# Kernel optimization log

Measured on AMD Instinct MI355X. Metric: run time of the kernel, lower is better.

## Reference

```python
import jax, jax.numpy as jnp
import numpy as np

NUM_HEADS = 6
EPS = 1e-05


def setup_inputs() -> dict:
    key = jax.random.key(0)
    k1, k2, k3 = jax.random.split(key, 3)
    B, N, C = 8, 1024, 384
    x = jax.random.normal(k1, (B, N, C), dtype=jnp.float32)
    Wqkv = jax.random.normal(k2, (3 * C, C), dtype=jnp.float32) * (1.0 / np.sqrt(C))
    Wproj = jax.random.normal(k3, (C, C), dtype=jnp.float32) * (1.0 / np.sqrt(C))
    bproj = jnp.zeros((C,), dtype=jnp.float32)
    alpha = jnp.ones((1, NUM_HEADS, 1, 1), dtype=jnp.float32)
    return {"x": x, "Wqkv": Wqkv, "Wproj": Wproj, "bproj": bproj, "alpha": alpha}


def reference(x, Wqkv, Wproj, bproj, alpha):
    B, N, C = x.shape
    H = NUM_HEADS
    hd = C // H
    scale = hd ** -0.5
    # qkv projection (torch Linear: x @ W^T), split into q,k,v of shape [B,H,N,hd]
    qkv = (x @ Wqkv.T).reshape(B, N, 3, H, hd).transpose(2, 0, 3, 1, 4)
    q, k, v = qkv[0], qkv[1], qkv[2]
    attn = jnp.einsum('bhqd,bhkd->bhqk', q, k) * scale  # [B,H,N,N]
    scalattn = attn / N  # divide by attn.size(3) == N
    a = jax.nn.relu(attn)
    a = a / (jnp.sum(a, axis=-1, keepdims=True) + EPS)
    attn = alpha * a + (1.0 - alpha) * scalattn
    out = jnp.einsum('bhqk,bhkd->bhqd', attn, v)  # [B,H,N,hd]
    out = out.transpose(0, 2, 1, 3).reshape(B, N, C)
    return out @ Wproj.T + bproj
```

## Files before the change

### kernel.cpp

```cpp
#include <hip/hip_runtime.h>
#include <stdint.h>

typedef _Float16 f16;
typedef _Float16 half8 __attribute__((ext_vector_type(8)));
typedef float f32x4 __attribute__((ext_vector_type(4)));

#define MFMA16(A, B, C) __builtin_amdgcn_mfma_f32_16x16x32_f16(A, B, C, 0, 0, 0)

#define GLOAD16(g, l) __builtin_amdgcn_global_load_lds( \
    (const __attribute__((address_space(1))) uint32_t*)(g), \
    (__attribute__((address_space(3))) uint32_t*)(l), 16, 0, 0)

__device__ inline uint32_t packh(f16 a, f16 b) {
    union { f16 h[2]; uint32_t u; } t;
    t.h[0] = a; t.h[1] = b;
    return t.u;
}

#define XE4 786432
#define WQ4 110592
#define WP4 36864

__global__ __launch_bounds__(256) void convert_all(
    const float* __restrict__ x, const float* __restrict__ wq,
    const float* __restrict__ wp, f16* __restrict__ xo,
    f16* __restrict__ wqo, f16* __restrict__ wpo) {
    const int total = XE4 + WQ4 + WP4;
    for (int i = blockIdx.x * blockDim.x + threadIdx.x; i < total;
         i += gridDim.x * blockDim.x) {
        const float* src;
        f16* dst;
        int idx = i;
        if (idx < XE4) { src = x; dst = xo; }
        else if (idx < XE4 + WQ4) { idx -= XE4; src = wq; dst = wqo; }
        else { idx -= XE4 + WQ4; src = wp; dst = wpo; }
        float4 v = ((const float4*)src)[idx];
        union { f16 x[4]; uint2 u; } H;
        H.x[0] = (f16)v.x; H.x[1] = (f16)v.y;
        H.x[2] = (f16)v.z; H.x[3] = (f16)v.w;
        ((uint2*)dst)[idx] = H.u;
    }
}

__global__ __launch_bounds__(256) void qkv_gemm(
    const f16* __restrict__ x16, const f16* __restrict__ w16,
    f16* __restrict__ q_, f16* __restrict__ k_, f16* __restrict__ vt_) {
    __shared__ f16 sA[3][4096], sB[3][4096];
    const int tid = threadIdx.x;
    const int w = tid >> 6, lane = tid & 63;
    const int g = lane >> 4, q = lane & 15;
    const int m0 = blockIdx.x * 128, j0 = blockIdx.y * 128;
    const int wm = (w >> 1) * 64, wn = (w & 1) * 64;
    const bool isV = (j0 >= 768);

    const char* gA = (const char*)x16 + (size_t)m0 * 768;
    const char* gB = (const char*)w16 + (size_t)j0 * 768;
    auto STAGE = [&](int buf, int ks) {
#pragma unroll
        for (int i = 0; i < 2; ++i) {
            const int r0 = 32 * w + i * 16;
            const int row = r0 + (lane >> 2);
            const int chs = ((lane & 3) ^ ((row & 6) >> 1)) << 4;
            GLOAD16(gA + (size_t)row * 768 + ks * 64 + chs, &sA[buf][r0 * 32]);
            GLOAD16(gB + (size_t)row * 768 + ks * 64 + chs, &sB[buf][r0 * 32]);
        }
    };

    f32x4 acc[4][4];
#pragma unroll
    for (int i = 0; i < 4; ++i)
#pragma unroll
        for (int j = 0; j < 4; ++j) acc[i][j] = (f32x4){0.f, 0.f, 0.f, 0.f};

    asm volatile("" ::: "memory");
    STAGE(0, 0);
    STAGE(1, 1);
    for (int ks = 0; ks < 12; ++ks) {
        const int cur = ks % 3;
        __builtin_amdgcn_s_barrier();
        if (ks < 10) {
            STAGE((ks + 2) % 3, ks + 2);
            asm volatile("s_waitcnt vmcnt(8)" ::: "memory");
        } else if (ks == 10) {
            asm volatile("s_waitcnt vmcnt(4)" ::: "memory");
        } else {
            asm volatile("s_waitcnt vmcnt(0)" ::: "memory");
        }
        __builtin_amdgcn_s_barrier();

        half8 am[4], bn[4];
#pragma unroll
        for (int mi = 0; mi < 4; ++mi) {
            const int row = wm + 16 * mi + q;
            const int ch = (g ^ ((row & 6) >> 1)) * 8;
            am[mi] = *(const half8*)&sA[cur][row * 32 + ch];
        }
#pragma unroll
        for (int nj = 0; nj < 4; ++nj) {
            const int row = wn + 16 * nj + q;
            const int ch = (g ^ ((row & 6) >> 1)) * 8;
            bn[nj] = *(const half8*)&sB[cur][row * 32 + ch];
        }
        __builtin_amdgcn_s_setprio(1);
        if (!isV) {
#pragma unroll
            for (int mi = 0; mi < 4; ++mi)
#pragma unroll
                for (int nj = 0; nj < 4; ++nj)
                    acc[mi][nj] = MFMA16(bn[nj], am[mi], acc[mi][nj]);
        } else {
#pragma unroll
            for (int mi = 0; mi < 4; ++mi)
#pragma unroll
                for (int nj = 0; nj < 4; ++nj)
                    acc[mi][nj] = MFMA16(am[mi], bn[nj], acc[mi][nj]);
        }
        __builtin_amdgcn_s_setprio(0);
    }

    if (!isV) {
        const int t = j0 / 384;
        const float sc = (t == 0) ? 0.125f : 1.0f;
        f16* dst = (t == 0) ? q_ : k_;
#pragma unroll
        for (int nj = 0; nj < 4; ++nj) {
            const int jb = j0 + wn + 16 * nj + 4 * g;
            const int h = (jb - t * 384) >> 6, d0 = jb & 63;
#pragma unroll
            for (int mi = 0; mi < 4; ++mi) {
                const int mg = m0 + wm + 16 * mi + q;
                const int b = mg >> 10, n = mg & 1023;
                const size_t base = (size_t)(b * 6 + h) * 65536 + (size_t)n * 64 + d0;
                union { f16 x[4]; uint2 u; } H;
#pragma unroll
                for (int r = 0; r < 4; ++r) H.x[r] = (f16)(acc[mi][nj][r] * sc);
                *(uint2*)&dst[base] = H.u;
            }
        }
    } else {
#pragma unroll
        for (int nj = 0; nj < 4; ++nj) {
            const int jc = j0 + wn + 16 * nj + q;
            const int h = (jc - 768) >> 6, d = jc & 63;
#pragma unroll
            for (int mi = 0; mi < 4; ++mi) {
                const int mg = m0 + wm + 16 * mi + 4 * g;
                const int b = mg >> 10, n = mg & 1023;
                const size_t bh = (size_t)(b * 6 + h);
                union { f16 x[4]; uint2 u; } HV;
#pragma unroll
                for (int r = 0; r < 4; ++r) HV.x[r] = (f16)acc[mi][nj][r];
                *(uint2*)&vt_[bh * 65536 + (size_t)d * 1024 + n] = HV.u;
            }
        }
    }
}

__global__ __launch_bounds__(512) void attn_mfma(
    const f16* __restrict__ q_, const f16* __restrict__ k_,
    const f16* __restrict__ vt_, const float* __restrict__ alpha,
    f16* __restrict__ ao_) {
    __shared__ f16 sK[2][4096], sV[2][4096];
    const int tid = threadIdx.x;
    const int w = tid >> 6, lane = tid & 63;
    const int g = lane >> 4, q = lane & 15;
    const int bh = blockIdx.x % 48, h = bh % 6;
    const int n0 = (blockIdx.x / 48) * 128;

    const size_t kbb = (size_t)bh * 131072;
    const int rl8 = lane >> 3, cl8 = lane & 7;

    auto STAGE = [&](int buf, int kt) {
        const size_t kb = kbb + (size_t)kt * 8192;
        const size_t vb = kbb + (size_t)kt * 128;
        const int rloc = 8 * w + rl8;
        const int chs = (cl8 ^ (rloc & 7)) << 4;
        const int ldso = 8 * w * 64;
        GLOAD16((const char*)k_ + kb + (size_t)rloc * 128 + chs, &sK[buf][ldso]);
        GLOAD16((const char*)vt_ + vb + (size_t)rloc * 2048 + chs, &sV[buf][ldso]);
    };

    const size_t qbase = (size_t)bh * 65536 + (size_t)(n0 + 16 * w + q) * 64;
    half8 Qh[2];
    Qh[0] = *(const half8*)&q_[qbase + g * 8];
    Qh[1] = *(const half8*)&q_[qbase + 32 + g * 8];
    const float al = alpha[h];
    const float cg = (1.0f - al) * (1.0f / 1024.0f);
    const bool useLin = (cg != 0.0f);

    f32x4 accP[4], accS[4];
#pragma unroll
    for (int i = 0; i < 4; ++i) {
        accP[i] = (f32x4){0.f, 0.f, 0.f, 0.f};
        accS[i] = (f32x4){0.f, 0.f, 0.f, 0.f};
    }
    float rs = 0.f;

    asm volatile("" ::: "memory");
    STAGE(0, 0);
    int cur = 0;
    for (int kt = 0; kt < 16; ++kt) {
        __builtin_amdgcn_s_barrier();
        if (kt < 15) {
            STAGE(cur ^ 1, kt + 1);
            asm volatile("s_waitcnt vmcnt(2)" ::: "memory");
        } else {
            asm volatile("s_waitcnt vmcnt(0)" ::: "memory");
        }
        __builtin_amdgcn_s_barrier();

        f32x4 sv[4];
        __builtin_amdgcn_s_setprio(1);
#pragma unroll
        for (int s = 0; s < 4; ++s) {
            f32x4 sa = (f32x4){0.f, 0.f, 0.f, 0.f};
            const int row = 16 * s + q;
#pragma unroll
            for (int k2 = 0; k2 < 2; ++k2) {
                const int ch = ((k2 * 4 + g) ^ (row & 7)) * 8;
                half8 kf = *(const half8*)&sK[cur][row * 64 + ch];
                sa = MFMA16(kf, Qh[k2], sa);
            }
            sv[s] = sa;
        }
        __builtin_amdgcn_s_setprio(0);

        uint32_t pk[4][2];
#pragma unroll
        for (int s = 0; s < 4; ++s) {
            float p0 = fmaxf(sv[s][0], 0.f), p1 = fmaxf(sv[s][1], 0.f);
            float p2 = fmaxf(sv[s][2], 0.f), p3 = fmaxf(sv[s][3], 0.f);
            rs += (p0 + p1) + (p2 + p3);
            pk[s][0] = packh((f16)p0, (f16)p1);
            pk[s][1] = packh((f16)p2, (f16)p3);
        }

#pragma unroll
        for (int t2 = 0; t2 < 2; ++t2) {
            union { uint32_t u[4]; half8 v; } fh;
#pragma unroll
            for (int r = 0; r < 4; ++r) {
                const int srcl = ((2 * g + (r >> 1)) & 3) * 16 + q;
                uint32_t a0 = __shfl(pk[2 * t2][r & 1], srcl, 64);
                uint32_t b0 = __shfl(pk[2 * t2 + 1][r & 1], srcl, 64);
                fh.u[r] = (g < 2) ? a0 : b0;
            }
            __builtin_amdgcn_s_setprio(1);
#pragma unroll
            for (int ds = 0; ds < 4; ++ds) {
                const int row = 16 * ds + q;
                const int ch = ((t2 * 4 + g) ^ (row & 7)) * 8;
                half8 vf = *(const half8*)&sV[cur][row * 64 + ch];
                accP[ds] = MFMA16(vf, fh.v, accP[ds]);
            }
            __builtin_amdgcn_s_setprio(0);
        }

        if (useLin) {
            uint32_t sk[4][2];
#pragma unroll
            for (int s = 0; s < 4; ++s) {
                sk[s][0] = packh((f16)sv[s][0], (f16)sv[s][1]);
                sk[s][1] = packh((f16)sv[s][2], (f16)sv[s][3]);
            }
#pragma unroll
            for (int t2 = 0; t2 < 2; ++t2) {
                union { uint32_t u[4]; half8 v; } fh;
#pragma unroll
                for (int r = 0; r < 4; ++r) {
                    const int srcl = ((2 * g + (r >> 1)) & 3) * 16 + q;
                    uint32_t a0 = __shfl(sk[2 * t2][r & 1], srcl, 64);
                    uint32_t b0 = __shfl(sk[2 * t2 + 1][r & 1], srcl, 64);
                    fh.u[r] = (g < 2) ? a0 : b0;
                }
#pragma unroll
                for (int ds = 0; ds < 4; ++ds) {
                    const int row = 16 * ds + q;
                    const int ch = ((t2 * 4 + g) ^ (row & 7)) * 8;
                    half8 vf = *(const half8*)&sV[cur][row * 64 + ch];
                    accS[ds] = MFMA16(vf, fh.v, accS[ds]);
                }
            }
        }
        cur ^= 1;
    }

    rs += __shfl_xor(rs, 16, 64);
    rs += __shfl_xor(rs, 32, 64);
    const float inv = al / (rs + 1e-5f);

    const int b = bh / 6;
    const size_t arow = (size_t)(b * 1024 + n0 + 16 * w + q) * 384 + h * 64;
#pragma unroll
    for (int ds = 0; ds < 4; ++ds) {
        const int d0 = 16 * ds + 4 * g;
        union { f16 x[4]; uint2 u; } H;
#pragma unroll
        for (int r = 0; r < 4; ++r)
            H.x[r] = (f16)(accP[ds][r] * inv + cg * accS[ds][r]);
        *(uint2*)&ao_[arow + d0] = H.u;
    }
}

__global__ __launch_bounds__(256) void proj_gemm(
    const f16* __restrict__ a_, const f16* __restrict__ wp16,
    const float* __restrict__ bias, float* __restrict__ out) {
    __shared__ f16 sA[3][2048], sB[3][4096];
    const int tid = threadIdx.x;
    const int w = tid >> 6, lane = tid & 63;
    const int g = lane >> 4, q = lane & 15;
    const int m0 = blockIdx.x * 64, j0 = blockIdx.y * 128;
    const int wm = (w >> 1) * 32, wn = (w & 1) * 64;

    const char* gA = (const char*)a_ + (size_t)m0 * 768;
    const char* gB = (const char*)wp16 + (size_t)j0 * 768;
    auto STAGE = [&](int buf, int ks) {
        {
            const int r0 = 16 * w;
            const int row = r0 + (lane >> 2);
            const int chs = ((lane & 3) ^ ((row & 6) >> 1)) << 4;
            GLOAD16(gA + (size_t)row * 768 + ks * 64 + chs, &sA[buf][r0 * 32]);
        }
#pragma unroll
        for (int i = 0; i < 2; ++i) {
            const int r0 = 32 * w + i * 16;
            const int row = r0 + (lane >> 2);
            const int chs = ((lane & 3) ^ ((row & 6) >> 1)) << 4;
            GLOAD16(gB + (size_t)row * 768 + ks * 64 + chs, &sB[buf][r0 * 32]);
        }
    };

    f32x4 acc[2][4];
#pragma unroll
    for (int i = 0; i < 2; ++i)
#pragma unroll
        for (int j = 0; j < 4; ++j) acc[i][j] = (f32x4){0.f, 0.f, 0.f, 0.f};

    asm volatile("" ::: "memory");
    STAGE(0, 0);
    STAGE(1, 1);
    for (int ks = 0; ks < 12; ++ks) {
        const int cur = ks % 3;
        __builtin_amdgcn_s_barrier();
        if (ks < 10) {
            STAGE((ks + 2) % 3, ks + 2);
            asm volatile("s_waitcnt vmcnt(6)" ::: "memory");
        } else if (ks == 10) {
            asm volatile("s_waitcnt vmcnt(3)" ::: "memory");
        } else {
            asm volatile("s_waitcnt vmcnt(0)" ::: "memory");
        }
        __builtin_amdgcn_s_barrier();

        half8 am[2], bn[4];
#pragma unroll
        for (int mi = 0; mi < 2; ++mi) {
            const int row = wm + 16 * mi + q;
            const int ch = (g ^ ((row & 6) >> 1)) * 8;
            am[mi] = *(const half8*)&sA[cur][row * 32 + ch];
        }
#pragma unroll
        for (int nj = 0; nj < 4; ++nj) {
            const int row = wn + 16 * nj + q;
            const int ch = (g ^ ((row & 6) >> 1)) * 8;
            bn[nj] = *(const half8*)&sB[cur][row * 32 + ch];
        }
        __builtin_amdgcn_s_setprio(1);
#pragma unroll
        for (int mi = 0; mi < 2; ++mi)
#pragma unroll
            for (int nj = 0; nj < 4; ++nj)
                acc[mi][nj] = MFMA16(bn[nj], am[mi], acc[mi][nj]);
        __builtin_amdgcn_s_setprio(0);
    }

#pragma unroll
    for (int nj = 0; nj < 4; ++nj) {
        const int jb = j0 + wn + 16 * nj + 4 * g;
        const float4 bb = *(const float4*)&bias[jb];
#pragma unroll
        for (int mi = 0; mi < 2; ++mi) {
            const int m = m0 + wm + 16 * mi + q;
            float4 o;
            o.x = acc[mi][nj][0] + bb.x;
            o.y = acc[mi][nj][1] + bb.y;
            o.z = acc[mi][nj][2] + bb.z;
            o.w = acc[mi][nj][3] + bb.w;
            *(float4*)&out[(size_t)m * 384 + jb] = o;
        }
    }
}

extern "C" void kernel_launch(void* const* d_in, const int* in_sizes, int n_in,
                              void* d_out, int out_size, void* d_ws, size_t ws_size,
                              hipStream_t stream) {
    const float* x     = (const float*)d_in[0];
    const float* Wqkv  = (const float*)d_in[1];
    const float* Wproj = (const float*)d_in[2];
    const float* bproj = (const float*)d_in[3];
    const float* alpha = (const float*)d_in[4];
    float* out = (float*)d_out;

    f16* ws = (f16*)d_ws;
    const size_t XE = 8192 * 384;
    const size_t WQ = 1152 * 384;
    const size_t WP = 384 * 384;
    const size_t QE = 48 * 1024 * 64;

    f16* x16  = ws;            f16* wq16 = x16 + XE;
    f16* wp16 = wq16 + WQ;
    f16* qv   = wp16 + WP;     f16* kv   = qv + QE;
    f16* vt   = kv + QE;       f16* ao   = vt + QE;

    convert_all<<<1024, 256, 0, stream>>>(x, Wqkv, Wproj, x16, wq16, wp16);
    qkv_gemm<<<dim3(64, 9), 256, 0, stream>>>(x16, wq16, qv, kv, vt);
    attn_mfma<<<384, 512, 0, stream>>>(qv, kv, vt, alpha, ao);
    proj_gemm<<<dim3(128, 3), 256, 0, stream>>>(ao, wp16, bproj, out);
}
```

Baseline: 134.9 us.

## Switch QKV and proj GEMMs to BK=64 double-buffered pipeline

Both GEMMs move from a 3-stage pipeline with a 32-wide K step to a 2-stage pipeline with a 64-wide K step. The LDS swizzle changes to an 8-chunk XOR pattern to match. This halves the number of barrier pairs and loop iterations per tile and doubles the MFMA work between syncs. The cost is shallower prefetch depth, which may leave more global-load latency exposed, plus more registers for the operand fragments.

```diff
diff --git a/kernel.cpp b/kernel.cpp
--- a/kernel.cpp
+++ b/kernel.cpp
@@ -45,7 +45,7 @@
 __global__ __launch_bounds__(256) void qkv_gemm(
     const f16* __restrict__ x16, const f16* __restrict__ w16,
     f16* __restrict__ q_, f16* __restrict__ k_, f16* __restrict__ vt_) {
-    __shared__ f16 sA[3][4096], sB[3][4096];
+    __shared__ f16 sA[2][8192], sB[2][8192];
     const int tid = threadIdx.x;
     const int w = tid >> 6, lane = tid & 63;
     const int g = lane >> 4, q = lane & 15;
@@ -57,12 +57,12 @@
     const char* gB = (const char*)w16 + (size_t)j0 * 768;
     auto STAGE = [&](int buf, int ks) {
 #pragma unroll
-        for (int i = 0; i < 2; ++i) {
-            const int r0 = 32 * w + i * 16;
-            const int row = r0 + (lane >> 2);
-            const int chs = ((lane & 3) ^ ((row & 6) >> 1)) << 4;
-            GLOAD16(gA + (size_t)row * 768 + ks * 64 + chs, &sA[buf][r0 * 32]);
-            GLOAD16(gB + (size_t)row * 768 + ks * 64 + chs, &sB[buf][r0 * 32]);
+        for (int i = 0; i < 4; ++i) {
+            const int r0 = 32 * w + i * 8;
+            const int row = r0 + (lane >> 3);
+            const int chs = ((lane & 7) ^ (row & 7)) << 4;
+            GLOAD16(gA + (size_t)row * 768 + ks * 128 + chs, &sA[buf][r0 * 64]);
+            GLOAD16(gB + (size_t)row * 768 + ks * 128 + chs, &sB[buf][r0 * 64]);
         }
     };
 
@@ -74,32 +74,35 @@
 
     asm volatile("" ::: "memory");
     STAGE(0, 0);
-    STAGE(1, 1);
-    for (int ks = 0; ks < 12; ++ks) {
-        const int cur = ks % 3;
-        __builtin_amdgcn_s_barrier();
-        if (ks < 10) {
-            STAGE((ks + 2) % 3, ks + 2);
+    int cur = 0;
+    for (int ks = 0; ks < 6; ++ks) {
+        __builtin_amdgcn_s_barrier();
+        if (ks < 5) {
+            STAGE(cur ^ 1, ks + 1);
             asm volatile("s_waitcnt vmcnt(8)" ::: "memory");
-        } else if (ks == 10) {
-            asm volatile("s_waitcnt vmcnt(4)" ::: "memory");
         } else {
             asm volatile("s_waitcnt vmcnt(0)" ::: "memory");
         }
         __builtin_amdgcn_s_barrier();
 
-        half8 am[4], bn[4];
+        half8 am[4][2], bn[4][2];
 #pragma unroll
         for (int mi = 0; mi < 4; ++mi) {
             const int row = wm + 16 * mi + q;
-            const int ch = (g ^ ((row & 6) >> 1)) * 8;
-            am[mi] = *(const half8*)&sA[cur][row * 32 + ch];
+#pragma unroll
+            for (int k2 = 0; k2 < 2; ++k2) {
+                const int ch = ((k2 * 4 + g) ^ (row & 7)) * 8;
+                am[mi][k2] = *(const half8*)&sA[cur][row * 64 + ch];
+            }
         }
 #pragma unroll
         for (int nj = 0; nj < 4; ++nj) {
             const int row = wn + 16 * nj + q;
-            const int ch = (g ^ ((row & 6) >> 1)) * 8;
-            bn[nj] = *(const half8*)&sB[cur][row * 32 + ch];
+#pragma unroll
+            for (int k2 = 0; k2 < 2; ++k2) {
+                const int ch = ((k2 * 4 + g) ^ (row & 7)) * 8;
+                bn[nj][k2] = *(const half8*)&sB[cur][row * 64 + ch];
+            }
         }
         __builtin_amdgcn_s_setprio(1);
         if (!isV) {
@@ -107,15 +110,20 @@
             for (int mi = 0; mi < 4; ++mi)
 #pragma unroll
                 for (int nj = 0; nj < 4; ++nj)
-                    acc[mi][nj] = MFMA16(bn[nj], am[mi], acc[mi][nj]);
+#pragma unroll
+                    for (int k2 = 0; k2 < 2; ++k2)
+                        acc[mi][nj] = MFMA16(bn[nj][k2], am[mi][k2], acc[mi][nj]);
         } else {
 #pragma unroll
             for (int mi = 0; mi < 4; ++mi)
 #pragma unroll
                 for (int nj = 0; nj < 4; ++nj)
-                    acc[mi][nj] = MFMA16(am[mi], bn[nj], acc[mi][nj]);
+#pragma unroll
+                    for (int k2 = 0; k2 < 2; ++k2)
+                        acc[mi][nj] = MFMA16(am[mi][k2], bn[nj][k2], acc[mi][nj]);
         }
         __builtin_amdgcn_s_setprio(0);
+        cur ^= 1;
     }
 
     if (!isV) {
@@ -305,7 +313,7 @@
 __global__ __launch_bounds__(256) void proj_gemm(
     const f16* __restrict__ a_, const f16* __restrict__ wp16,
     const float* __restrict__ bias, float* __restrict__ out) {
-    __shared__ f16 sA[3][2048], sB[3][4096];
+    __shared__ f16 sA[2][4096], sB[2][8192];
     const int tid = threadIdx.x;
     const int w = tid >> 6, lane = tid & 63;
     const int g = lane >> 4, q = lane & 15;
@@ -315,18 +323,19 @@
     const char* gA = (const char*)a_ + (size_t)m0 * 768;
     const char* gB = (const char*)wp16 + (size_t)j0 * 768;
     auto STAGE = [&](int buf, int ks) {
-        {
-            const int r0 = 16 * w;
-            const int row = r0 + (lane >> 2);
-            const int chs = ((lane & 3) ^ ((row & 6) >> 1)) << 4;
-            GLOAD16(gA + (size_t)row * 768 + ks * 64 + chs, &sA[buf][r0 * 32]);
-        }
 #pragma unroll
         for (int i = 0; i < 2; ++i) {
-            const int r0 = 32 * w + i * 16;
-            const int row = r0 + (lane >> 2);
-            const int chs = ((lane & 3) ^ ((row & 6) >> 1)) << 4;
-            GLOAD16(gB + (size_t)row * 768 + ks * 64 + chs, &sB[buf][r0 * 32]);
+            const int r0 = 16 * w + i * 8;
+            const int row = r0 + (lane >> 3);
+            const int chs = ((lane & 7) ^ (row & 7)) << 4;
+            GLOAD16(gA + (size_t)row * 768 + ks * 128 + chs, &sA[buf][r0 * 64]);
+        }
+#pragma unroll
+        for (int i = 0; i < 4; ++i) {
+            const int r0 = 32 * w + i * 8;
+            const int row = r0 + (lane >> 3);
+            const int chs = ((lane & 7) ^ (row & 7)) << 4;
+            GLOAD16(gB + (size_t)row * 768 + ks * 128 + chs, &sB[buf][r0 * 64]);
         }
     };
 
@@ -338,40 +347,46 @@
 
     asm volatile("" ::: "memory");
     STAGE(0, 0);
-    STAGE(1, 1);
-    for (int ks = 0; ks < 12; ++ks) {
-        const int cur = ks % 3;
-        __builtin_amdgcn_s_barrier();
-        if (ks < 10) {
-            STAGE((ks + 2) % 3, ks + 2);
+    int cur = 0;
+    for (int ks = 0; ks < 6; ++ks) {
+        __builtin_amdgcn_s_barrier();
+        if (ks < 5) {
+            STAGE(cur ^ 1, ks + 1);
             asm volatile("s_waitcnt vmcnt(6)" ::: "memory");
-        } else if (ks == 10) {
-            asm volatile("s_waitcnt vmcnt(3)" ::: "memory");
         } else {
             asm volatile("s_waitcnt vmcnt(0)" ::: "memory");
         }
         __builtin_amdgcn_s_barrier();
 
-        half8 am[2], bn[4];
+        half8 am[2][2], bn[4][2];
 #pragma unroll
         for (int mi = 0; mi < 2; ++mi) {
             const int row = wm + 16 * mi + q;
-            const int ch = (g ^ ((row & 6) >> 1)) * 8;
-            am[mi] = *(const half8*)&sA[cur][row * 32 + ch];
+#pragma unroll
+            for (int k2 = 0; k2 < 2; ++k2) {
+                const int ch = ((k2 * 4 + g) ^ (row & 7)) * 8;
+                am[mi][k2] = *(const half8*)&sA[cur][row * 64 + ch];
+            }
         }
 #pragma unroll
         for (int nj = 0; nj < 4; ++nj) {
             const int row = wn + 16 * nj + q;
-            const int ch = (g ^ ((row & 6) >> 1)) * 8;
-            bn[nj] = *(const half8*)&sB[cur][row * 32 + ch];
+#pragma unroll
+            for (int k2 = 0; k2 < 2; ++k2) {
+                const int ch = ((k2 * 4 + g) ^ (row & 7)) * 8;
+                bn[nj][k2] = *(const half8*)&sB[cur][row * 64 + ch];
+            }
         }
         __builtin_amdgcn_s_setprio(1);
 #pragma unroll
         for (int mi = 0; mi < 2; ++mi)
 #pragma unroll
             for (int nj = 0; nj < 4; ++nj)
-                acc[mi][nj] = MFMA16(bn[nj], am[mi], acc[mi][nj]);
+#pragma unroll
+                for (int k2 = 0; k2 < 2; ++k2)
+                    acc[mi][nj] = MFMA16(bn[nj][k2], am[mi][k2], acc[mi][nj]);
         __builtin_amdgcn_s_setprio(0);
+        cur ^= 1;
     }
 
 #pragma unroll
```

After: 131.6 us. 2.5% less time.
